# Optimization experiments

Measured on AMD Instinct MI355X. Metric: run time of the kernel, lower is better.

Reference implementation:

```python
import jax, jax.numpy as jnp
import numpy as np

N_WIRES = 4
DEPTH = 2
BN_EPS = 1e-5


def _rx(theta):
    c = jnp.cos(theta / 2).astype(jnp.complex64)
    s = jnp.sin(theta / 2).astype(jnp.complex64)
    return jnp.stack([jnp.stack([c, -1j * s], -1),
                      jnp.stack([-1j * s, c], -1)], -2)


def _ry(theta):
    c = jnp.cos(theta / 2).astype(jnp.complex64)
    s = jnp.sin(theta / 2).astype(jnp.complex64)
    return jnp.stack([jnp.stack([c, -s], -1),
                      jnp.stack([s, c], -1)], -2)


def _rz(theta):
    e = jnp.exp(-1j * theta.astype(jnp.complex64) / 2)
    z = jnp.zeros_like(e)
    return jnp.stack([jnp.stack([e, z], -1),
                      jnp.stack([z, jnp.conj(e)], -1)], -2)


def _apply_1q(state, U, wire):
    # state: [B,2,2,2,2]; U: [2,2] (shared) or [B,2,2] (per-sample)
    ax = 1 + wire
    st = jnp.moveaxis(state, ax, -1)
    if U.ndim == 3:
        st = jnp.einsum('bij,b...j->b...i', U, st)
    else:
        st = jnp.einsum('ij,...j->...i', U, st)
    return jnp.moveaxis(st, -1, ax)


def _apply_cnot(state, c, t):
    axc, axt = 1 + c, 1 + t
    st = jnp.moveaxis(state, (axc, axt), (-2, -1))
    st = jnp.stack([st[..., 0, :], st[..., 1, ::-1]], axis=-2)
    return jnp.moveaxis(st, (-2, -1), (axc, axt))


def _circuit(pooled, enc_w, enc_b, var_params):
    B = pooled.shape[0]
    angles = pooled @ enc_w.T + enc_b  # [B,4]
    # |0000> state, [B,2,2,2,2]
    state = jnp.zeros((B, 16), jnp.complex64).at[:, 0].set(1.0)
    state = state.reshape((B,) + (2,) * N_WIRES)
    for i in range(N_WIRES):
        state = _apply_1q(state, _rx(angles[:, i]), i)  # batched RX encoding
    for d in range(DEPTH):
        for i in range(N_WIRES):
            state = _apply_1q(state, _rx(var_params[d, i, 0]), i)
            state = _apply_1q(state, _ry(var_params[d, i, 1]), i)
            state = _apply_1q(state, _rz(var_params[d, i, 2]), i)
        for i in range(N_WIRES - 1):
            state = _apply_cnot(state, i, i + 1)
        state = _apply_cnot(state, N_WIRES - 1, 0)
    probs = jnp.real(state * jnp.conj(state))  # [B,2,2,2,2]
    zs = []
    for i in range(N_WIRES):
        other = tuple(a for a in range(1, 1 + N_WIRES) if a != 1 + i)
        p = probs.sum(other)  # [B,2]
        zs.append(p[:, 0] - p[:, 1])
    return jnp.stack(zs, -1)  # [B,4]


def setup_inputs() -> dict:
    key = jax.random.key(0)
    ks = jax.random.split(key, 4)
    B = 65536
    return {
        'x': jax.random.normal(ks[0], (B, 1, 24, 24), jnp.float32),
        'enc_w': jax.random.normal(ks[1], (4, 16), jnp.float32) * 0.25,
        'enc_b': jax.random.normal(ks[2], (4,), jnp.float32) * 0.25,
        'var_params': jax.random.normal(ks[3], (DEPTH, N_WIRES, 3), jnp.float32),
        'gamma': jnp.ones((4,), jnp.float32),
        'beta': jnp.zeros((4,), jnp.float32),
    }


def reference(x, enc_w, enc_b, var_params, gamma, beta):
    B = x.shape[0]
    # avg_pool2d kernel 6 on [B,1,24,24] -> [B,1,4,4] -> [B,16]
    pooled = x.reshape(B, 1, 4, 6, 4, 6).mean((3, 5)).reshape(B, 16)
    z = _circuit(pooled, enc_w, enc_b, var_params)  # [B,4] analytic expvals
    # BatchNorm1d (training mode: biased batch statistics)
    mean = z.mean(0)
    var = z.var(0)
    return (z - mean) / jnp.sqrt(var + BN_EPS) * gamma + beta
```

## Files before the change

### kernel.cpp

```cpp
#include <hip/hip_runtime.h>


__device__ __forceinline__ void apply_rx(float* sr, float* si, int bit, float c, float s) {
    const int m = 1 << bit;
#pragma unroll
    for (int idx = 0; idx < 16; ++idx) {
        if (idx & m) continue;
        const int j = idx | m;
        float a0r = sr[idx], a0i = si[idx], a1r = sr[j], a1i = si[j];
        sr[idx] = c * a0r + s * a1i;
        si[idx] = c * a0i - s * a1r;
        sr[j]   = c * a1r + s * a0i;
        si[j]   = c * a1i - s * a0r;
    }
}

__device__ __forceinline__ void apply_ry(float* sr, float* si, int bit, float c, float s) {
    const int m = 1 << bit;
#pragma unroll
    for (int idx = 0; idx < 16; ++idx) {
        if (idx & m) continue;
        const int j = idx | m;
        float a0r = sr[idx], a0i = si[idx], a1r = sr[j], a1i = si[j];
        sr[idx] = c * a0r - s * a1r;
        si[idx] = c * a0i - s * a1i;
        sr[j]   = s * a0r + c * a1r;
        si[j]   = s * a0i + c * a1i;
    }
}

__device__ __forceinline__ void apply_rz(float* sr, float* si, int bit, float c, float s) {
    const int m = 1 << bit;
#pragma unroll
    for (int idx = 0; idx < 16; ++idx) {
        if (idx & m) continue;
        const int j = idx | m;
        float a0r = sr[idx], a0i = si[idx], a1r = sr[j], a1i = si[j];
        sr[idx] = c * a0r + s * a0i;
        si[idx] = c * a0i - s * a0r;
        sr[j]   = c * a1r - s * a1i;
        si[j]   = c * a1i + s * a1r;
    }
}

__device__ __forceinline__ void apply_cnot(float* sr, float* si, int cw, int tw) {
    const int cb = 3 - cw, tb = 3 - tw;
#pragma unroll
    for (int idx = 0; idx < 16; ++idx) {
        if (((idx >> cb) & 1) && !((idx >> tb) & 1)) {
            const int j = idx | (1 << tb);
            float tr = sr[idx]; sr[idx] = sr[j]; sr[j] = tr;
            float ti = si[idx]; si[idx] = si[j]; si[j] = ti;
        }
    }
}


__global__ __launch_bounds__(256) void pool_angles_kernel(
    const float4* __restrict__ x,
    const float* __restrict__ enc_w,
    const float* __restrict__ enc_b,
    float* __restrict__ angles_out)
{
    __shared__ float4 xbuf[8 * 144];
    __shared__ float pooled[8][17];

    const int t = threadIdx.x;
    const int blk = blockIdx.x;

    const float4* src = x + (size_t)blk * 1152;
#pragma unroll
    for (int j = 0; j < 4; ++j)
        xbuf[t + 256 * j] = src[t + 256 * j];
    if (t < 128)
        xbuf[1024 + t] = src[1024 + t];
    __syncthreads();

    {
        const int s = t >> 5;
        const int q = t & 31;
        const int cell = q & 15;
        const int half = q >> 4;
        const int pr = cell >> 2, pc = cell & 3;
        const float* sb = reinterpret_cast<const float*>(xbuf) + s * 576;
        const int base = pr * 144 + pc * 6 + half * 72;
        float acc = 0.0f;
#pragma unroll
        for (int r0 = 0; r0 < 3; ++r0) {
            int r = r0 + (pr & 3);
            if (r >= 3) r -= 3;
            const int rowbase = base + r * 24;
#pragma unroll
            for (int c = 0; c < 6; ++c)
                acc += sb[rowbase + c];
        }
        acc += __shfl_xor(acc, 16, 64);
        if (half == 0)
            pooled[s][cell] = acc * (1.0f / 36.0f);
    }
    __syncthreads();

    if (t < 32) {
        const int s = t >> 2, i = t & 3;
        float a = enc_b[i];
#pragma unroll
        for (int k = 0; k < 16; ++k)
            a += enc_w[i * 16 + k] * pooled[s][k];
        angles_out[(blk * 8 + s) * 4 + i] = a;
    }
}

__global__ __launch_bounds__(256) void circuit_kernel(
    float4* __restrict__ io,
    const float* __restrict__ var_params,
    float* __restrict__ partials)
{
    __shared__ float gc[24], gs[24];
    __shared__ float red[4 * 8];

    const int t = threadIdx.x;
    if (t < 24) {
        float th = 0.5f * var_params[t];
        float s, c;
        __sincosf(th, &s, &c);
        gc[t] = c; gs[t] = s;
    }
    __syncthreads();

    const int b = blockIdx.x * 256 + t;
    const float4 a4 = io[b];
    const float av[4] = {a4.x, a4.y, a4.z, a4.w};

    float sr[16], si[16];
#pragma unroll
    for (int i = 0; i < 16; ++i) { sr[i] = 0.0f; si[i] = 0.0f; }
    sr[0] = 1.0f;

#pragma unroll
    for (int w = 0; w < 4; ++w) {
        float s, c;
        __sincosf(0.5f * av[w], &s, &c);
        apply_rx(sr, si, 3 - w, c, s);
    }

#pragma unroll
    for (int d = 0; d < 2; ++d) {
#pragma unroll
        for (int w = 0; w < 4; ++w) {
            const int base = d * 12 + w * 3;
            apply_rx(sr, si, 3 - w, gc[base + 0], gs[base + 0]);
            apply_ry(sr, si, 3 - w, gc[base + 1], gs[base + 1]);
            apply_rz(sr, si, 3 - w, gc[base + 2], gs[base + 2]);
        }
        apply_cnot(sr, si, 0, 1);
        apply_cnot(sr, si, 1, 2);
        apply_cnot(sr, si, 2, 3);
        apply_cnot(sr, si, 3, 0);
    }

    float pr16[16];
#pragma unroll
    for (int i = 0; i < 16; ++i) pr16[i] = sr[i] * sr[i] + si[i] * si[i];

    float z[4];
#pragma unroll
    for (int w = 0; w < 4; ++w) {
        const int bit = 3 - w;
        float acc = 0.0f;
#pragma unroll
        for (int i = 0; i < 16; ++i)
            acc += ((i >> bit) & 1) ? -pr16[i] : pr16[i];
        z[w] = acc;
    }

    io[b] = make_float4(z[0], z[1], z[2], z[3]);

    float vals[8] = {z[0], z[1], z[2], z[3],
                     z[0] * z[0], z[1] * z[1], z[2] * z[2], z[3] * z[3]};
#pragma unroll
    for (int j = 0; j < 8; ++j) {
        float v = vals[j];
#pragma unroll
        for (int off = 32; off >= 1; off >>= 1)
            v += __shfl_down(v, off, 64);
        if ((t & 63) == 0) red[(t >> 6) * 8 + j] = v;
    }
    __syncthreads();
    if (t < 8) {
        partials[blockIdx.x * 8 + t] = red[t] + red[8 + t] + red[16 + t] + red[24 + t];
    }
}

__global__ __launch_bounds__(256) void bn_kernel(
    float4* __restrict__ io,
    const float* __restrict__ partials,
    const float* __restrict__ gamma,
    const float* __restrict__ beta,
    int nPartialRows, int B)
{
    __shared__ float stats[8];
    const int t = threadIdx.x;

    if (t < 64) {
        float part[8];
#pragma unroll
        for (int j = 0; j < 8; ++j) part[j] = 0.0f;
        for (int r = t; r < nPartialRows; r += 64) {
            const float* row = partials + r * 8;
#pragma unroll
            for (int j = 0; j < 8; ++j) part[j] += row[j];
        }
#pragma unroll
        for (int j = 0; j < 8; ++j) {
            float v = part[j];
#pragma unroll
            for (int off = 32; off >= 1; off >>= 1)
                v += __shfl_down(v, off, 64);
            if (t == 0) stats[j] = v;
        }
    }
    __syncthreads();

    const int b = blockIdx.x * 256 + t;
    const float invB = 1.0f / (float)B;
    const float4 z4 = io[b];
    const float zz[4] = {z4.x, z4.y, z4.z, z4.w};

    float res[4];
#pragma unroll
    for (int i = 0; i < 4; ++i) {
        const float mean = stats[i] * invB;
        float var = stats[4 + i] * invB - mean * mean;
        var = fmaxf(var, 0.0f);
        const float scale = gamma[i] * rsqrtf(var + 1e-5f);
        res[i] = (zz[i] - mean) * scale + beta[i];
    }
    io[b] = make_float4(res[0], res[1], res[2], res[3]);
}

extern "C" void kernel_launch(void* const* d_in, const int* in_sizes, int n_in,
                              void* d_out, int out_size, void* d_ws, size_t ws_size,
                              hipStream_t stream) {
    const float4* x = (const float4*)d_in[0];
    const float* enc_w = (const float*)d_in[1];
    const float* enc_b = (const float*)d_in[2];
    const float* var_params = (const float*)d_in[3];
    const float* gamma = (const float*)d_in[4];
    const float* beta = (const float*)d_in[5];

    const int B = in_sizes[0] / 576;
    float* io = (float*)d_out;
    float* partials = (float*)d_ws;

    const int nCircuitBlocks = B / 256;

    pool_angles_kernel<<<B / 8, 256, 0, stream>>>(x, enc_w, enc_b, io);
    circuit_kernel<<<nCircuitBlocks, 256, 0, stream>>>((float4*)io, var_params, partials);
    bn_kernel<<<nCircuitBlocks, 256, 0, stream>>>((float4*)io, partials, gamma, beta,
                                                  nCircuitBlocks, B);
}
```

Baseline: 227.0 us.

## Fuse pooling, circuit and batchnorm into one cooperative grid-synced kernel

Replaces the three-kernel pipeline (pool+angles, circuit, batchnorm) with a single cooperative kernel. Each thread pools its own sample straight from global memory into registers, runs the circuit, writes per-block partial statistics, then waits on a grid-wide sync before normalising and writing the output. This drops two launches and the round trip of angles and z values through global memory. The cost is that the input read changes from coalesced block-wide shared-memory staging to strided per-thread 2.3KB reads, and only B/256 blocks of 256 threads run, giving low occupancy for a memory-bound phase. The cooperative launch also needs every block to be resident at once.

Result: slower. 295.4 us (+30.1%).

```diff
diff --git a/kernel.cpp b/kernel.cpp
--- a/kernel.cpp
+++ b/kernel.cpp
@@ -1,4 +1,7 @@
 #include <hip/hip_runtime.h>
+#include <hip/hip_cooperative_groups.h>
+
+namespace cg = cooperative_groups;
 
 
 __device__ __forceinline__ void apply_rx(float* sr, float* si, int bit, float c, float s) {
@@ -56,80 +59,56 @@
 }
 
 
-__global__ __launch_bounds__(256) void pool_angles_kernel(
+__global__ __launch_bounds__(256) void fused_kernel(
     const float4* __restrict__ x,
     const float* __restrict__ enc_w,
     const float* __restrict__ enc_b,
-    float* __restrict__ angles_out)
+    const float* __restrict__ var_params,
+    const float* __restrict__ gamma,
+    const float* __restrict__ beta,
+    float4* __restrict__ out,
+    float* __restrict__ partials,
+    int B)
 {
-    __shared__ float4 xbuf[8 * 144];
-    __shared__ float pooled[8][17];
+    __shared__ float red[4 * 8];
+    __shared__ float stats[8];
 
     const int t = threadIdx.x;
-    const int blk = blockIdx.x;
-
-    const float4* src = x + (size_t)blk * 1152;
-#pragma unroll
-    for (int j = 0; j < 4; ++j)
-        xbuf[t + 256 * j] = src[t + 256 * j];
-    if (t < 128)
-        xbuf[1024 + t] = src[1024 + t];
-    __syncthreads();
-
-    {
-        const int s = t >> 5;
-        const int q = t & 31;
-        const int cell = q & 15;
-        const int half = q >> 4;
-        const int pr = cell >> 2, pc = cell & 3;
-        const float* sb = reinterpret_cast<const float*>(xbuf) + s * 576;
-        const int base = pr * 144 + pc * 6 + half * 72;
-        float acc = 0.0f;
-#pragma unroll
-        for (int r0 = 0; r0 < 3; ++r0) {
-            int r = r0 + (pr & 3);
-            if (r >= 3) r -= 3;
-            const int rowbase = base + r * 24;
-#pragma unroll
-            for (int c = 0; c < 6; ++c)
-                acc += sb[rowbase + c];
-        }
-        acc += __shfl_xor(acc, 16, 64);
-        if (half == 0)
-            pooled[s][cell] = acc * (1.0f / 36.0f);
-    }
-    __syncthreads();
-
-    if (t < 32) {
-        const int s = t >> 2, i = t & 3;
+    const int s = blockIdx.x * 256 + t;
+
+    float pooled[16];
+#pragma unroll
+    for (int i = 0; i < 16; ++i) pooled[i] = 0.0f;
+
+    const float4* xs = x + (size_t)s * 144;
+#pragma unroll
+    for (int k = 0; k < 144; ++k) {
+        const float4 v = xs[k];
+        { const int f = 4 * k + 0, r = f / 24, c = f - 24 * r; pooled[(r / 6) * 4 + (c / 6)] += v.x; }
+        { const int f = 4 * k + 1, r = f / 24, c = f - 24 * r; pooled[(r / 6) * 4 + (c / 6)] += v.y; }
+        { const int f = 4 * k + 2, r = f / 24, c = f - 24 * r; pooled[(r / 6) * 4 + (c / 6)] += v.z; }
+        { const int f = 4 * k + 3, r = f / 24, c = f - 24 * r; pooled[(r / 6) * 4 + (c / 6)] += v.w; }
+    }
+#pragma unroll
+    for (int i = 0; i < 16; ++i) pooled[i] *= (1.0f / 36.0f);
+
+    float av[4];
+#pragma unroll
+    for (int i = 0; i < 4; ++i) {
         float a = enc_b[i];
 #pragma unroll
         for (int k = 0; k < 16; ++k)
-            a += enc_w[i * 16 + k] * pooled[s][k];
-        angles_out[(blk * 8 + s) * 4 + i] = a;
-    }
-}
-
-__global__ __launch_bounds__(256) void circuit_kernel(
-    float4* __restrict__ io,
-    const float* __restrict__ var_params,
-    float* __restrict__ partials)
-{
-    __shared__ float gc[24], gs[24];
-    __shared__ float red[4 * 8];
-
-    const int t = threadIdx.x;
-    if (t < 24) {
-        float th = 0.5f * var_params[t];
-        float s, c;
-        __sincosf(th, &s, &c);
-        gc[t] = c; gs[t] = s;
-    }
-    __syncthreads();
-
-    const int b = blockIdx.x * 256 + t;
-    const float4 a4 = io[b];
-    const float av[4] = {a4.x, a4.y, a4.z, a4.w};
+            a += enc_w[i * 16 + k] * pooled[k];
+        av[i] = a;
+    }
+
+    float gc[24], gs[24];
+#pragma unroll
+    for (int i = 0; i < 24; ++i) {
+        float sn, cs;
+        __sincosf(0.5f * var_params[i], &sn, &cs);
+        gc[i] = cs; gs[i] = sn;
+    }
 
     float sr[16], si[16];
 #pragma unroll
@@ -138,9 +117,9 @@
 
 #pragma unroll
     for (int w = 0; w < 4; ++w) {
-        float s, c;
-        __sincosf(0.5f * av[w], &s, &c);
-        apply_rx(sr, si, 3 - w, c, s);
+        float sn, cs;
+        __sincosf(0.5f * av[w], &sn, &cs);
+        apply_rx(sr, si, 3 - w, cs, sn);
     }
 
 #pragma unroll
@@ -173,8 +152,6 @@
         z[w] = acc;
     }
 
-    io[b] = make_float4(z[0], z[1], z[2], z[3]);
-
     float vals[8] = {z[0], z[1], z[2], z[3],
                      z[0] * z[0], z[1] * z[1], z[2] * z[2], z[3] * z[3]};
 #pragma unroll
@@ -186,26 +163,17 @@
         if ((t & 63) == 0) red[(t >> 6) * 8 + j] = v;
     }
     __syncthreads();
-    if (t < 8) {
+    if (t < 8)
         partials[blockIdx.x * 8 + t] = red[t] + red[8 + t] + red[16 + t] + red[24 + t];
-    }
-}
-
-__global__ __launch_bounds__(256) void bn_kernel(
-    float4* __restrict__ io,
-    const float* __restrict__ partials,
-    const float* __restrict__ gamma,
-    const float* __restrict__ beta,
-    int nPartialRows, int B)
-{
-    __shared__ float stats[8];
-    const int t = threadIdx.x;
+
+    __threadfence();
+    cg::this_grid().sync();
 
     if (t < 64) {
         float part[8];
 #pragma unroll
         for (int j = 0; j < 8; ++j) part[j] = 0.0f;
-        for (int r = t; r < nPartialRows; r += 64) {
+        for (int r = t; r < (int)gridDim.x; r += 64) {
             const float* row = partials + r * 8;
 #pragma unroll
             for (int j = 0; j < 8; ++j) part[j] += row[j];
@@ -221,11 +189,7 @@
     }
     __syncthreads();
 
-    const int b = blockIdx.x * 256 + t;
     const float invB = 1.0f / (float)B;
-    const float4 z4 = io[b];
-    const float zz[4] = {z4.x, z4.y, z4.z, z4.w};
-
     float res[4];
 #pragma unroll
     for (int i = 0; i < 4; ++i) {
@@ -233,9 +197,9 @@
         float var = stats[4 + i] * invB - mean * mean;
         var = fmaxf(var, 0.0f);
         const float scale = gamma[i] * rsqrtf(var + 1e-5f);
-        res[i] = (zz[i] - mean) * scale + beta[i];
-    }
-    io[b] = make_float4(res[0], res[1], res[2], res[3]);
+        res[i] = (z[i] - mean) * scale + beta[i];
+    }
+    out[s] = make_float4(res[0], res[1], res[2], res[3]);
 }
 
 extern "C" void kernel_launch(void* const* d_in, const int* in_sizes, int n_in,
@@ -248,14 +212,15 @@
     const float* gamma = (const float*)d_in[4];
     const float* beta = (const float*)d_in[5];
 
-    const int B = in_sizes[0] / 576;
-    float* io = (float*)d_out;
+    int B = in_sizes[0] / 576;
+    float4* out = (float4*)d_out;
     float* partials = (float*)d_ws;
 
-    const int nCircuitBlocks = B / 256;
-
-    pool_angles_kernel<<<B / 8, 256, 0, stream>>>(x, enc_w, enc_b, io);
-    circuit_kernel<<<nCircuitBlocks, 256, 0, stream>>>((float4*)io, var_params, partials);
-    bn_kernel<<<nCircuitBlocks, 256, 0, stream>>>((float4*)io, partials, gamma, beta,
-                                                  nCircuitBlocks, B);
-}
+    int nBlocks = B / 256;
+
+    void* args[] = {(void*)&x, (void*)&enc_w, (void*)&enc_b, (void*)&var_params,
+                    (void*)&gamma, (void*)&beta, (void*)&out, (void*)&partials,
+                    (void*)&B};
+    hipLaunchCooperativeKernel((const void*)fused_kernel, dim3(nBlocks), dim3(256),
+                               args, 0, stream);
+}
```

## Fuse circuit and batchnorm via cooperative grid sync; async global-to-LDS loads

Applied to the files above, without the earlier changes.

Merges the circuit and BatchNorm kernels into one cooperative kernel that writes per-block partial sums, synchronises the whole grid, then reduces the stats and normalises z kept in registers. This removes a kernel launch and a round trip of z through global memory. The pooling kernel now uses global_load_lds to copy input straight into LDS, skipping the register staging. The risk is grid-sync cost, plus the fallback to two kernels when 256 blocks cannot all be co-resident.

Result: slower. 279.2 us (+23.0%).

```diff
diff --git a/kernel.cpp b/kernel.cpp
--- a/kernel.cpp
+++ b/kernel.cpp
@@ -1,4 +1,7 @@
 #include <hip/hip_runtime.h>
+#include <hip/hip_cooperative_groups.h>
+
+namespace cg = cooperative_groups;
 
 
 __device__ __forceinline__ void apply_rx(float* sr, float* si, int bit, float c, float s) {
@@ -70,10 +73,18 @@
 
     const float4* src = x + (size_t)blk * 1152;
 #pragma unroll
-    for (int j = 0; j < 4; ++j)
-        xbuf[t + 256 * j] = src[t + 256 * j];
-    if (t < 128)
-        xbuf[1024 + t] = src[1024 + t];
+    for (int j = 0; j < 4; ++j) {
+        __builtin_amdgcn_global_load_lds(
+            (const __attribute__((address_space(1))) void*)(src + t + 256 * j),
+            (__attribute__((address_space(3))) void*)(&xbuf[t + 256 * j]),
+            16, 0, 0);
+    }
+    if (t < 128) {
+        __builtin_amdgcn_global_load_lds(
+            (const __attribute__((address_space(1))) void*)(src + 1024 + t),
+            (__attribute__((address_space(3))) void*)(&xbuf[1024 + t]),
+            16, 0, 0);
+    }
     __syncthreads();
 
     {
@@ -110,6 +121,122 @@
     }
 }
 
+__global__ __launch_bounds__(256) void circuit_bn_coop(
+    float4* __restrict__ io,
+    const float* __restrict__ var_params,
+    const float* __restrict__ gamma,
+    const float* __restrict__ beta,
+    float* __restrict__ partials,
+    int B)
+{
+    __shared__ float gc[24], gs[24];
+    __shared__ float red[4 * 8];
+    __shared__ float stats[8];
+
+    const int t = threadIdx.x;
+    if (t < 24) {
+        float th = 0.5f * var_params[t];
+        float s, c;
+        __sincosf(th, &s, &c);
+        gc[t] = c; gs[t] = s;
+    }
+    __syncthreads();
+
+    const int b = blockIdx.x * 256 + t;
+    const float4 a4 = io[b];
+    const float av[4] = {a4.x, a4.y, a4.z, a4.w};
+
+    float sr[16], si[16];
+#pragma unroll
+    for (int i = 0; i < 16; ++i) { sr[i] = 0.0f; si[i] = 0.0f; }
+    sr[0] = 1.0f;
+
+#pragma unroll
+    for (int w = 0; w < 4; ++w) {
+        float s, c;
+        __sincosf(0.5f * av[w], &s, &c);
+        apply_rx(sr, si, 3 - w, c, s);
+    }
+
+#pragma unroll
+    for (int d = 0; d < 2; ++d) {
+#pragma unroll
+        for (int w = 0; w < 4; ++w) {
+            const int base = d * 12 + w * 3;
+            apply_rx(sr, si, 3 - w, gc[base + 0], gs[base + 0]);
+            apply_ry(sr, si, 3 - w, gc[base + 1], gs[base + 1]);
+            apply_rz(sr, si, 3 - w, gc[base + 2], gs[base + 2]);
+        }
+        apply_cnot(sr, si, 0, 1);
+        apply_cnot(sr, si, 1, 2);
+        apply_cnot(sr, si, 2, 3);
+        apply_cnot(sr, si, 3, 0);
+    }
+
+    float pr16[16];
+#pragma unroll
+    for (int i = 0; i < 16; ++i) pr16[i] = sr[i] * sr[i] + si[i] * si[i];
+
+    float z[4];
+#pragma unroll
+    for (int w = 0; w < 4; ++w) {
+        const int bit = 3 - w;
+        float acc = 0.0f;
+#pragma unroll
+        for (int i = 0; i < 16; ++i)
+            acc += ((i >> bit) & 1) ? -pr16[i] : pr16[i];
+        z[w] = acc;
+    }
+
+    float vals[8] = {z[0], z[1], z[2], z[3],
+                     z[0] * z[0], z[1] * z[1], z[2] * z[2], z[3] * z[3]};
+#pragma unroll
+    for (int j = 0; j < 8; ++j) {
+        float v = vals[j];
+#pragma unroll
+        for (int off = 32; off >= 1; off >>= 1)
+            v += __shfl_down(v, off, 64);
+        if ((t & 63) == 0) red[(t >> 6) * 8 + j] = v;
+    }
+    __syncthreads();
+    if (t < 8)
+        partials[blockIdx.x * 8 + t] = red[t] + red[8 + t] + red[16 + t] + red[24 + t];
+
+    __threadfence();
+    cg::this_grid().sync();
+
+    const int nRows = (int)gridDim.x;
+    if (t < 64) {
+        float part[8] = {0, 0, 0, 0, 0, 0, 0, 0};
+        for (int r = t; r < nRows; r += 64) {
+            const float* row = partials + r * 8;
+#pragma unroll
+            for (int j = 0; j < 8; ++j) part[j] += row[j];
+        }
+#pragma unroll
+        for (int j = 0; j < 8; ++j) {
+            float v = part[j];
+#pragma unroll
+            for (int off = 32; off >= 1; off >>= 1)
+                v += __shfl_down(v, off, 64);
+            if (t == 0) stats[j] = v;
+        }
+    }
+    __syncthreads();
+
+    const float invB = 1.0f / (float)B;
+    float res[4];
+#pragma unroll
+    for (int i = 0; i < 4; ++i) {
+        const float mean = stats[i] * invB;
+        float var = stats[4 + i] * invB - mean * mean;
+        var = fmaxf(var, 0.0f);
+        const float scale = gamma[i] * rsqrtf(var + 1e-5f);
+        res[i] = (z[i] - mean) * scale + beta[i];
+    }
+    io[b] = make_float4(res[0], res[1], res[2], res[3]);
+}
+
 __global__ __launch_bounds__(256) void circuit_kernel(
     float4* __restrict__ io,
     const float* __restrict__ var_params,
@@ -186,9 +313,8 @@
         if ((t & 63) == 0) red[(t >> 6) * 8 + j] = v;
     }
     __syncthreads();
-    if (t < 8) {
+    if (t < 8)
         partials[blockIdx.x * 8 + t] = red[t] + red[8 + t] + red[16 + t] + red[24 + t];
-    }
 }
 
 __global__ __launch_bounds__(256) void bn_kernel(
@@ -248,14 +374,33 @@
     const float* gamma = (const float*)d_in[4];
     const float* beta = (const float*)d_in[5];
 
-    const int B = in_sizes[0] / 576;
+    int B = in_sizes[0] / 576;
     float* io = (float*)d_out;
     float* partials = (float*)d_ws;
 
     const int nCircuitBlocks = B / 256;
 
+    static int mode = -1;
+    if (mode < 0) {
+        int maxActive = 0;
+        hipError_t e = hipOccupancyMaxActiveBlocksPerMultiprocessor(
+            &maxActive, circuit_bn_coop, 256, 0);
+        int numCU = 0;
+        hipDeviceGetAttribute(&numCU, hipDeviceAttributeMultiprocessorCount, 0);
+        mode = (e == hipSuccess && numCU > 0 && maxActive * numCU >= nCircuitBlocks) ? 1 : 0;
+    }
+
     pool_angles_kernel<<<B / 8, 256, 0, stream>>>(x, enc_w, enc_b, io);
-    circuit_kernel<<<nCircuitBlocks, 256, 0, stream>>>((float4*)io, var_params, partials);
-    bn_kernel<<<nCircuitBlocks, 256, 0, stream>>>((float4*)io, partials, gamma, beta,
-                                                  nCircuitBlocks, B);
-}
+
+    if (mode == 1) {
+        float4* io4 = (float4*)io;
+        void* args[] = {(void*)&io4, (void*)&var_params, (void*)&gamma, (void*)&beta,
+                        (void*)&partials, (void*)&B};
+        hipLaunchCooperativeKernel((const void*)circuit_bn_coop, dim3(nCircuitBlocks),
+                                   dim3(256), args, 0, stream);
+    } else {
+        circuit_kernel<<<nCircuitBlocks, 256, 0, stream>>>((float4*)io, var_params, partials);
+        bn_kernel<<<nCircuitBlocks, 256, 0, stream>>>((float4*)io, partials, gamma, beta,
+                                                      nCircuitBlocks, B);
+    }
+}
```

## Double-buffer pooling tiles with direct global-to-LDS async loads

Applied to the files above, without the earlier changes.

The pooling kernel now processes two 8-sample tiles per block. Both tiles are loaded with global_load_lds, which writes global data straight into LDS without a register round trip. Pooling of the first tile starts as soon as its loads complete, while the second tile's loads are still in flight. The intent is to overlap memory latency with compute on this bandwidth-bound stage, at the cost of twice the LDS per block, which can lower occupancy, and hand-written waitcnt and barrier ordering that must be kept correct.

New measurement: 227.7 us. Within noise of the previous version (+0.3%).

```diff
diff --git a/kernel.cpp b/kernel.cpp
--- a/kernel.cpp
+++ b/kernel.cpp
@@ -55,34 +55,26 @@
     }
 }
 
-
-__global__ __launch_bounds__(256) void pool_angles_kernel(
-    const float4* __restrict__ x,
+#define GLLDS(gp, lp)                                                          \
+    __builtin_amdgcn_global_load_lds(                                          \
+        (const __attribute__((address_space(1))) void*)(gp),                   \
+        (__attribute__((address_space(3))) void*)(lp), 16, 0, 0)
+
+__device__ __forceinline__ void pool_tile_angles(
+    const float4* __restrict__ xbuf_tile,
+    float (*pooled)[17],
     const float* __restrict__ enc_w,
     const float* __restrict__ enc_b,
-    float* __restrict__ angles_out)
-{
-    __shared__ float4 xbuf[8 * 144];
-    __shared__ float pooled[8][17];
-
-    const int t = threadIdx.x;
-    const int blk = blockIdx.x;
-
-    const float4* src = x + (size_t)blk * 1152;
-#pragma unroll
-    for (int j = 0; j < 4; ++j)
-        xbuf[t + 256 * j] = src[t + 256 * j];
-    if (t < 128)
-        xbuf[1024 + t] = src[1024 + t];
-    __syncthreads();
-
+    float* __restrict__ angles_out,
+    int sampleBase, int t)
+{
     {
         const int s = t >> 5;
         const int q = t & 31;
         const int cell = q & 15;
         const int half = q >> 4;
         const int pr = cell >> 2, pc = cell & 3;
-        const float* sb = reinterpret_cast<const float*>(xbuf) + s * 576;
+        const float* sb = reinterpret_cast<const float*>(xbuf_tile) + s * 576;
         const int base = pr * 144 + pc * 6 + half * 72;
         float acc = 0.0f;
 #pragma unroll
@@ -98,7 +90,9 @@
         if (half == 0)
             pooled[s][cell] = acc * (1.0f / 36.0f);
     }
-    __syncthreads();
+    asm volatile("s_waitcnt lgkmcnt(0)" ::: "memory");
+    __builtin_amdgcn_sched_barrier(0);
+    __builtin_amdgcn_s_barrier();
 
     if (t < 32) {
         const int s = t >> 2, i = t & 3;
@@ -106,8 +100,49 @@
 #pragma unroll
         for (int k = 0; k < 16; ++k)
             a += enc_w[i * 16 + k] * pooled[s][k];
-        angles_out[(blk * 8 + s) * 4 + i] = a;
-    }
+        angles_out[(sampleBase + s) * 4 + i] = a;
+    }
+}
+
+__global__ __launch_bounds__(256) void pool_angles_db(
+    const float4* __restrict__ x,
+    const float* __restrict__ enc_w,
+    const float* __restrict__ enc_b,
+    float* __restrict__ angles_out)
+{
+    __shared__ float4 xbuf[2][1152];
+    __shared__ float pooled[8][17];
+
+    const int t = threadIdx.x;
+    const int blk = blockIdx.x;
+    const float4* srcA = x + (size_t)blk * 2304;
+    const float4* srcB = srcA + 1152;
+
+#pragma unroll
+    for (int j = 0; j < 4; ++j)
+        GLLDS(srcA + t + 256 * j, &xbuf[0][t + 256 * j]);
+    if (t < 128)
+        GLLDS(srcA + 1024 + t, &xbuf[0][1024 + t]);
+    __builtin_amdgcn_sched_barrier(0);
+
+#pragma unroll
+    for (int j = 0; j < 4; ++j)
+        GLLDS(srcB + t + 256 * j, &xbuf[1][t + 256 * j]);
+    if (t < 128)
+        GLLDS(srcB + 1024 + t, &xbuf[1][1024 + t]);
+    __builtin_amdgcn_sched_barrier(0);
+
+    asm volatile("s_waitcnt vmcnt(4)" ::: "memory");
+    __builtin_amdgcn_sched_barrier(0);
+    __builtin_amdgcn_s_barrier();
+
+    pool_tile_angles(xbuf[0], pooled, enc_w, enc_b, angles_out, blk * 16, t);
+
+    asm volatile("s_waitcnt vmcnt(0)" ::: "memory");
+    __builtin_amdgcn_sched_barrier(0);
+    __builtin_amdgcn_s_barrier();
+
+    pool_tile_angles(xbuf[1], pooled, enc_w, enc_b, angles_out, blk * 16 + 8, t);
 }
 
 __global__ __launch_bounds__(256) void circuit_kernel(
@@ -186,9 +221,8 @@
         if ((t & 63) == 0) red[(t >> 6) * 8 + j] = v;
     }
     __syncthreads();
-    if (t < 8) {
+    if (t < 8)
         partials[blockIdx.x * 8 + t] = red[t] + red[8 + t] + red[16 + t] + red[24 + t];
-    }
 }
 
 __global__ __launch_bounds__(256) void bn_kernel(
@@ -254,7 +288,7 @@
 
     const int nCircuitBlocks = B / 256;
 
-    pool_angles_kernel<<<B / 8, 256, 0, stream>>>(x, enc_w, enc_b, io);
+    pool_angles_db<<<B / 16, 256, 0, stream>>>(x, enc_w, enc_b, io);
     circuit_kernel<<<nCircuitBlocks, 256, 0, stream>>>((float4*)io, var_params, partials);
     bn_kernel<<<nCircuitBlocks, 256, 0, stream>>>((float4*)io, partials, gamma, beta,
                                                   nCircuitBlocks, B);
```
